# Optimization experiments

Hardware: AMD Instinct MI355X
Metric: run time of the kernel (lower is better)

## Reference

```python
import jax, jax.numpy as jnp
import numpy as np

H = 16  # num_heads
D = 64  # head_dim (latent_dim // num_heads)


def setup_inputs() -> dict:
    key = jax.random.key(0)
    ks = jax.random.split(key, 14)
    B, L, S = 2, 1024, 4096
    input_dim, latent_dim, latent_rank = 2048, 1024, 128
    sc = 0.02
    return {
        "latent": jax.random.normal(ks[0], (B, L, latent_dim), jnp.float32),
        "x": jax.random.normal(ks[1], (B, S, input_dim), jnp.float32),
        "Wq": jax.random.normal(ks[2], (latent_dim, latent_dim), jnp.float32) * sc,
        "bq": jnp.zeros((latent_dim,), jnp.float32),
        "Wc": jax.random.normal(ks[3], (input_dim, latent_rank), jnp.float32) * sc,
        "bc": jnp.zeros((latent_rank,), jnp.float32),
        "Wk": jax.random.normal(ks[4], (latent_rank, latent_dim), jnp.float32) * sc,
        "bk": jnp.zeros((latent_dim,), jnp.float32),
        "Wv": jax.random.normal(ks[5], (latent_rank, latent_dim), jnp.float32) * sc,
        "bv": jnp.zeros((latent_dim,), jnp.float32),
        "Wo": jax.random.normal(ks[6], (latent_dim, latent_dim), jnp.float32) * sc,
        "bo": jnp.zeros((latent_dim,), jnp.float32),
    }


def reference(latent, x, Wq, bq, Wc, bc, Wk, bk, Wv, bv, Wo, bo):
    B, L, latent_dim = latent.shape
    S = x.shape[1]
    # projections
    Q = latent @ Wq + bq                      # [B, L, latent_dim]
    compressed = x @ Wc + bc                  # [B, S, latent_rank] low-rank latent
    K_full = compressed @ Wk + bk             # [B, S, latent_dim]
    V_full = compressed @ Wv + bv             # [B, S, latent_dim]
    # split heads -> [B, H, len, D]
    Qh = Q.reshape(B, L, H, D).transpose(0, 2, 1, 3)
    Kh = K_full.reshape(B, S, H, D).transpose(0, 2, 1, 3)
    Vh = V_full.reshape(B, S, H, D).transpose(0, 2, 1, 3)
    scale = 1.0 / jnp.sqrt(jnp.float32(D))
    scores = jnp.einsum("bhld,bhsd->bhls", Qh, Kh) * scale  # [B,H,L,S]
    attn = jax.nn.softmax(scores, axis=-1)
    ctx = jnp.einsum("bhls,bhsd->bhld", attn, Vh)            # [B,H,L,D]
    ctx = ctx.transpose(0, 2, 1, 3).reshape(B, L, latent_dim)
    return ctx @ Wo + bo
```

## Files before the change

kernel.cpp:

```cpp
#include <hip/hip_runtime.h>
#include <hip/hip_bf16.h>

using bf16x8  = __attribute__((ext_vector_type(8))) short;
using ushort8 = __attribute__((ext_vector_type(8))) unsigned short;
using f32x4   = __attribute__((ext_vector_type(4))) float;

#define DEVINL __device__ __forceinline__

DEVINL unsigned short f2bf(float f) {
    unsigned u = __builtin_bit_cast(unsigned, f);
    u += 0x7FFFu + ((u >> 16) & 1u);
    return (unsigned short)(u >> 16);
}

DEVINL void gload_lds16(const void* g, void* l) {
    __builtin_amdgcn_global_load_lds(
        (const __attribute__((address_space(1))) void*)g,
        (__attribute__((address_space(3))) void*)l, 16, 0, 0);
}

__global__ __launch_bounds__(256) void k_convTall(
        const float* __restrict__ Wq, const float* __restrict__ Wo,
        const float* __restrict__ Wk, const float* __restrict__ Wv,
        const float* __restrict__ Wc,
        unsigned short* __restrict__ WqT, unsigned short* __restrict__ WoT,
        unsigned short* __restrict__ WkT, unsigned short* __restrict__ WvT,
        unsigned short* __restrict__ WcT) {
    __shared__ float t[32][33];
    int bx = blockIdx.x;
    const float* in; unsigned short* out; int R, C, tix;
    if (bx < 1024)      { in = Wq; out = WqT; R = 1024; C = 1024; tix = bx; }
    else if (bx < 2048) { in = Wo; out = WoT; R = 1024; C = 1024; tix = bx - 1024; }
    else if (bx < 2176) { in = Wk; out = WkT; R = 128;  C = 1024; tix = bx - 2048; }
    else if (bx < 2304) { in = Wv; out = WvT; R = 128;  C = 1024; tix = bx - 2176; }
    else                { in = Wc; out = WcT; R = 2048; C = 128;  tix = bx - 2304; }
    int ctiles = C >> 5;
    int c0 = (tix % ctiles) * 32, r0 = (tix / ctiles) * 32;
    int tx = threadIdx.x, ty = threadIdx.y;
#pragma unroll
    for (int i = 0; i < 4; i++)
        t[ty + i * 8][tx] = in[(size_t)(r0 + ty + i * 8) * C + c0 + tx];
    __syncthreads();
#pragma unroll
    for (int i = 0; i < 4; i++)
        out[(size_t)(c0 + ty + i * 8) * R + r0 + tx] = f2bf(t[tx][ty + i * 8]);
}

template <int BM, int BN, int OUTBF, int BIASROW, int AMODE>
__global__ __launch_bounds__(256) void k_gemm(const void* __restrict__ Ain,
                                              const unsigned short* __restrict__ BT,
                                              const float* __restrict__ bias,
                                              void* __restrict__ Cout,
                                              int M, int N, int K, float scale,
                                              size_t zA, size_t zB, size_t zC,
                                              const float2* __restrict__ ML) {
    constexpr int WM = BM / 2, WN = BN / 2, MI = WM / 16, NI = WN / 16;
    constexpr int CB = BN * 8 / 256;
    constexpr int CA = BM * 8 / 256;
    constexpr int EPT = BM * 64 / 256;
    constexpr int TPR = 64 / EPT;
    constexpr int NAREG = (AMODE == 2) ? EPT / 2 : (AMODE == 1 ? EPT / 4 : 1);
    __shared__ unsigned short ls[2][(BM + BN) * 64];
    const int tid = threadIdx.x, lane = tid & 63, w = tid >> 6;
    const int m0 = blockIdx.y * BM, n0 = blockIdx.x * BN, zz = blockIdx.z;
    const int mw = (w >> 1) * WM, nw = (w & 1) * WN;
    const int r16 = lane & 15, g4 = lane >> 4;
    const unsigned short* A16 = (const unsigned short*)Ain + zA * zz;
    const float* A32 = (const float*)Ain;
    BT += zB * zz;
    const int arow = tid / TPR, acol = (tid % TPR) * EPT;

    float4 areg[NAREG];
    float2 mle[2];

    f32x4 acc[MI][NI];
#pragma unroll
    for (int a = 0; a < MI; a++)
#pragma unroll
        for (int b = 0; b < NI; b++) acc[a][b] = (f32x4){0.f, 0.f, 0.f, 0.f};

    auto LOAD_A = [&](int bufi, int k0) {
        if constexpr (AMODE == 0) {
#pragma unroll
            for (int i = 0; i < CA; i++) {
                int ch = i * 256 + w * 64 + lane;
                int row = ch >> 3, c = ch & 7;
                gload_lds16(A16 + (size_t)(m0 + row) * K + k0 + c * 8,
                            &ls[bufi][(size_t)(i * 256 + w * 64) * 8]);
            }
        } else if constexpr (AMODE == 1) {
            const float* src = A32 + (size_t)(m0 + arow) * K + k0 + acol;
#pragma unroll
            for (int j = 0; j < EPT / 4; j++) areg[j] = *(const float4*)(src + j * 4);
        } else {
            const float* src = A32 + (size_t)(m0 + arow) * K + k0 + acol;
#pragma unroll
            for (int j = 0; j < EPT / 4; j++) {
                areg[j] = *(const float4*)(src + j * 4);
                areg[j + EPT / 4] = *(const float4*)(src + 2097152 + j * 4);
            }
            int b = (m0 + arow) >> 10, q = (m0 + arow) & 1023, h = k0 >> 6;
            mle[0] = ML[((size_t)(b * 16 + h)) * 1024 + q];
            mle[1] = ML[((size_t)((2 + b) * 16 + h)) * 1024 + q];
        }
    };

    auto WRITE_A = [&](int bufi) {
        if constexpr (AMODE == 1) {
            unsigned u[EPT / 2];
#pragma unroll
            for (int j = 0; j < EPT / 4; j++) {
                asm("v_cvt_pk_bf16_f32 %0, %1, %2"
                    : "=v"(u[2 * j]) : "v"(areg[j].x), "v"(areg[j].y));
                asm("v_cvt_pk_bf16_f32 %0, %1, %2"
                    : "=v"(u[2 * j + 1]) : "v"(areg[j].z), "v"(areg[j].w));
            }
#pragma unroll
            for (int j = 0; j < EPT / 8; j++)
                *(uint4*)&ls[bufi][arow * 64 + acol + j * 8] =
                    make_uint4(u[4 * j], u[4 * j + 1], u[4 * j + 2], u[4 * j + 3]);
        } else if constexpr (AMODE == 2) {
            float Mx = fmaxf(mle[0].x, mle[1].x);
            float w0 = __builtin_amdgcn_exp2f(mle[0].x - Mx);
            float w1 = __builtin_amdgcn_exp2f(mle[1].x - Mx);
            float inv = 1.f / (w0 * mle[0].y + w1 * mle[1].y);
            w0 *= inv; w1 *= inv;
            unsigned u[EPT / 2];
#pragma unroll
            for (int j = 0; j < EPT / 4; j++) {
                float4 a = areg[j], c = areg[j + EPT / 4];
                float v0 = w0 * a.x + w1 * c.x, v1 = w0 * a.y + w1 * c.y;
                float v2 = w0 * a.z + w1 * c.z, v3 = w0 * a.w + w1 * c.w;
                asm("v_cvt_pk_bf16_f32 %0, %1, %2" : "=v"(u[2 * j]) : "v"(v0), "v"(v1));
                asm("v_cvt_pk_bf16_f32 %0, %1, %2" : "=v"(u[2 * j + 1]) : "v"(v2), "v"(v3));
            }
#pragma unroll
            for (int j = 0; j < EPT / 8; j++)
                *(uint4*)&ls[bufi][arow * 64 + acol + j * 8] =
                    make_uint4(u[4 * j], u[4 * j + 1], u[4 * j + 2], u[4 * j + 3]);
        }
    };

    auto STAGE_B = [&](int bufi, int k0) {
        unsigned short* lsB = &ls[bufi][BM * 64];
#pragma unroll
        for (int i = 0; i < CB; i++) {
            int ch = i * 256 + w * 64 + lane;
            int row = ch >> 3, c = ch & 7;
            gload_lds16(BT + (size_t)(n0 + row) * K + k0 + c * 8,
                        lsB + (size_t)(i * 256 + w * 64) * 8);
        }
    };

    auto COMPUTE = [&](int bufi) {
        const unsigned short* lsA = ls[bufi];
        const unsigned short* lsB = &ls[bufi][BM * 64];
#pragma unroll
        for (int kk = 0; kk < 2; kk++) {
            bf16x8 af[MI], bfr[NI];
#pragma unroll
            for (int a = 0; a < MI; a++)
                af[a] = *(const bf16x8*)&lsA[(mw + a * 16 + r16) * 64 + kk * 32 + g4 * 8];
#pragma unroll
            for (int b = 0; b < NI; b++)
                bfr[b] = *(const bf16x8*)&lsB[(nw + b * 16 + r16) * 64 + kk * 32 + g4 * 8];
#pragma unroll
            for (int a = 0; a < MI; a++)
#pragma unroll
                for (int b = 0; b < NI; b++)
                    acc[a][b] = __builtin_amdgcn_mfma_f32_16x16x32_bf16(af[a], bfr[b], acc[a][b], 0, 0, 0);
        }
    };

    const int nk = K >> 6;
    LOAD_A(0, 0);
    STAGE_B(0, 0);
    if constexpr (AMODE != 0) WRITE_A(0);
    __syncthreads();
    for (int t = 0; t < nk; ++t) {
        int cur = t & 1, nxt = cur ^ 1;
        if (t + 1 < nk) { LOAD_A(nxt, (t + 1) << 6); STAGE_B(nxt, (t + 1) << 6); }
        COMPUTE(cur);
        if (AMODE != 0 && t + 1 < nk) WRITE_A(nxt);
        __syncthreads();
    }

#pragma unroll
    for (int b = 0; b < NI; b++) {
        int col = n0 + nw + b * 16 + r16;
        float bvc = BIASROW ? 0.f : bias[col];
#pragma unroll
        for (int a = 0; a < MI; a++) {
#pragma unroll
            for (int r = 0; r < 4; r++) {
                int row = m0 + mw + a * 16 + g4 * 4 + r;
                float bv = BIASROW ? bias[row] : bvc;
                float v = (acc[a][b][r] + bv) * scale;
                if (OUTBF)
                    ((unsigned short*)Cout)[zC * zz + (size_t)row * N + col] = f2bf(v);
                else
                    ((float*)Cout)[zC * zz + (size_t)row * N + col] = v;
            }
        }
    }
}

__global__ __launch_bounds__(256, 4) void k_attn(const unsigned short* __restrict__ Qb,
                                                 const unsigned short* __restrict__ Kb,
                                                 const unsigned short* __restrict__ VTb,
                                                 float* __restrict__ ctxp,
                                                 float2* __restrict__ ML) {
    constexpr int LD = 1024;
    constexpr float MFIX = 4.0f;
    __shared__ unsigned short lsK[2][64 * 64];
    __shared__ unsigned short lsVT[2][64 * 64];
    __shared__ unsigned short lsP[4][16 * 64];
    const int tid = threadIdx.x, lane = tid & 63, w = tid >> 6;
    const int r16 = lane & 15, g4 = lane >> 4;
    const int wg = blockIdx.x;
    const int xcd = wg & 7, t_ = wg >> 3, qi = t_ & 15, gg = t_ >> 4;
    const int g = gg * 8 + xcd;
    const int bh = g & 31, z = g >> 5;
    const int b = bh >> 4, h = bh & 15;
    const int q0 = qi * 64 + w * 16;

    const size_t qbase = ((size_t)b * 1024 + q0 + r16) * LD + h * 64;
    bf16x8 qa0 = *(const bf16x8*)&Qb[qbase + g4 * 8];
    bf16x8 qa1 = *(const bf16x8*)&Qb[qbase + 32 + g4 * 8];

    f32x4 ctxa[4];
#pragma unroll
    for (int d = 0; d < 4; d++) ctxa[d] = (f32x4){0.f, 0.f, 0.f, 0.f};
    float l_run = 0.f;

    const int s7 = r16 & 7;
    const int offk0 = r16 * 64 + ((g4 ^ s7) << 3);
    const int offk1 = r16 * 64 + (((g4 + 4) ^ s7) << 3);
    const int pwb = r16 * 64 + (g4 & 1) * 4;
    const int c2 = g4 >> 1;
    const int swn[4] = {((0 + c2) ^ s7) << 3, ((2 + c2) ^ s7) << 3,
                        ((4 + c2) ^ s7) << 3, ((6 + c2) ^ s7) << 3};

    const int lrow = lane >> 3, lcol = lane & 7;
    const int csrc = lcol ^ lrow;
    const unsigned short* gK = Kb + (size_t)b * 4096 * LD + h * 64 +
                               (size_t)(w * 8 + lrow) * LD + csrc * 8;
    const unsigned short* gV = VTb + (size_t)bh * 64 * 4096 +
                               (size_t)(w * 8 + lrow) * 4096 + csrc * 8;

    auto STAGE = [&](int bufi, int s0) {
        gload_lds16(gK + (size_t)s0 * LD, &lsK[bufi][(w * 8) * 64]);
        gload_lds16(gK + (size_t)(s0 + 32) * LD, &lsK[bufi][(32 + w * 8) * 64]);
        gload_lds16(gV + s0, &lsVT[bufi][(w * 8) * 64]);
        gload_lds16(gV + s0 + 32 * 4096, &lsVT[bufi][(32 + w * 8) * 64]);
    };

    auto COMPUTE = [&](int bufi) {
        f32x4 sc[4];
#pragma unroll
        for (int ni = 0; ni < 4; ni++) sc[ni] = (f32x4){0.f, 0.f, 0.f, 0.f};
        __builtin_amdgcn_s_setprio(1);
#pragma unroll
        for (int kk = 0; kk < 2; kk++) {
            bf16x8 qa = kk ? qa1 : qa0;
            int ofk = kk ? offk1 : offk0;
#pragma unroll
            for (int ni = 0; ni < 4; ni++) {
                bf16x8 kf = *(const bf16x8*)&lsK[bufi][ni * 1024 + ofk];
                sc[ni] = __builtin_amdgcn_mfma_f32_16x16x32_bf16(kf, qa, sc[ni], 0, 0, 0);
            }
        }
        __builtin_amdgcn_s_setprio(0);

        float pl[4];
#pragma unroll
        for (int ni = 0; ni < 4; ni++) {
            float p0 = __builtin_amdgcn_exp2f(sc[ni][0] - MFIX);
            float p1 = __builtin_amdgcn_exp2f(sc[ni][1] - MFIX);
            float p2 = __builtin_amdgcn_exp2f(sc[ni][2] - MFIX);
            float p3 = __builtin_amdgcn_exp2f(sc[ni][3] - MFIX);
            pl[ni] = (p0 + p1) + (p2 + p3);
            unsigned u0, u1;
            asm("v_cvt_pk_bf16_f32 %0, %1, %2" : "=v"(u0) : "v"(p0), "v"(p1));
            asm("v_cvt_pk_bf16_f32 %0, %1, %2" : "=v"(u1) : "v"(p2), "v"(p3));
            *(uint2*)&lsP[w][pwb + swn[ni]] = make_uint2(u0, u1);
        }
        l_run += (pl[0] + pl[1]) + (pl[2] + pl[3]);

        __builtin_amdgcn_s_setprio(1);
#pragma unroll
        for (int kk = 0; kk < 2; kk++) {
            int ofk = kk ? offk1 : offk0;
            bf16x8 pa = *(const bf16x8*)&lsP[w][ofk];
#pragma unroll
            for (int di = 0; di < 4; di++) {
                bf16x8 vf = *(const bf16x8*)&lsVT[bufi][di * 1024 + ofk];
                ctxa[di] = __builtin_amdgcn_mfma_f32_16x16x32_bf16(pa, vf, ctxa[di], 0, 0, 0);
            }
        }
        __builtin_amdgcn_s_setprio(0);
    };

    const int t0 = z * 32, t1 = t0 + 32;
    STAGE(0, t0 * 64);
    __syncthreads();
#pragma unroll 1
    for (int t = t0; t < t1; ++t) {
        int cur = (t - t0) & 1;
        if (t + 1 < t1) STAGE(cur ^ 1, (t + 1) * 64);
        COMPUTE(cur);
        __syncthreads();
    }

    l_run += __shfl_xor(l_run, 16);
    l_run += __shfl_xor(l_run, 32);

    float* cp = ctxp + ((size_t)z * 2 + b) * 1024 * 1024;
#pragma unroll
    for (int r = 0; r < 4; r++) {
        int q = q0 + g4 * 4 + r;
#pragma unroll
        for (int di = 0; di < 4; di++)
            cp[(size_t)q * 1024 + h * 64 + di * 16 + r16] = ctxa[di][r];
    }
    if (g4 == 0)
        ML[(((size_t)z * 2 + b) * 16 + h) * 1024 + q0 + r16] = make_float2(MFIX, l_run);
}

extern "C" void kernel_launch(void* const* d_in, const int* in_sizes, int n_in,
                              void* d_out, int out_size, void* d_ws, size_t ws_size,
                              hipStream_t stream) {
    const float* latent = (const float*)d_in[0];
    const float* x      = (const float*)d_in[1];
    const float* Wq     = (const float*)d_in[2];
    const float* bq     = (const float*)d_in[3];
    const float* Wc     = (const float*)d_in[4];
    const float* bc     = (const float*)d_in[5];
    const float* Wk     = (const float*)d_in[6];
    const float* bk     = (const float*)d_in[7];
    const float* Wv     = (const float*)d_in[8];
    const float* bv     = (const float*)d_in[9];
    const float* Wo     = (const float*)d_in[10];
    const float* bo     = (const float*)d_in[11];
    float* out = (float*)d_out;

    char* ws = (char*)d_ws;
    size_t off = 0;
    auto alloc = [&](size_t shorts) {
        void* p = ws + off;
        off += (shorts * 2 + 255) & ~(size_t)255;
        return (unsigned short*)p;
    };
    unsigned short* WqT  = alloc(1048576);
    unsigned short* WcT  = alloc(262144);
    unsigned short* WkT  = alloc(131072);
    unsigned short* WvT  = alloc(131072);
    unsigned short* WoT  = alloc(1048576);
    unsigned short* comp = alloc(1048576);
    unsigned short* Qb   = alloc(2097152);
    unsigned short* Kb   = alloc(8388608);
    unsigned short* VTb  = alloc(8388608);
    float*          ctxp = (float*)alloc(8388608);
    float2*         MLp  = (float2*)alloc(262144);

    k_convTall<<<2560, dim3(32, 8), 0, stream>>>(Wq, Wo, Wk, Wv, Wc,
                                                 WqT, WoT, WkT, WvT, WcT);
    k_gemm<32, 128, 1, 0, 1><<<dim3(1, 256, 1), 256, 0, stream>>>(
        x, WcT, bc, comp, 8192, 128, 2048, 1.f, 0, 0, 0, nullptr);
    k_gemm<64, 64, 1, 0, 1><<<dim3(16, 32, 1), 256, 0, stream>>>(
        latent, WqT, bq, Qb, 2048, 1024, 1024, 0.18033688f, 0, 0, 0, nullptr);
    k_gemm<128, 128, 1, 0, 0><<<dim3(8, 64, 1), 256, 0, stream>>>(
        comp, WkT, bk, Kb, 8192, 1024, 128, 1.f, 0, 0, 0, nullptr);
    k_gemm<64, 64, 1, 1, 0><<<dim3(64, 16, 2), 256, 0, stream>>>(
        WvT, comp, bv, VTb, 1024, 4096, 128, 1.f,
        0, (size_t)4096 * 128, (size_t)16 * 64 * 4096, nullptr);
    k_attn<<<1024, 256, 0, stream>>>(Qb, Kb, VTb, ctxp, MLp);
    k_gemm<64, 64, 0, 0, 2><<<dim3(16, 32, 1), 256, 0, stream>>>(
        ctxp, WoT, bo, out, 2048, 1024, 1024, 1.f, 0, 0, 0, MLp);
}
```

Before: 275.4 us.

## Use 32x32x16 MFMA in attention with register-shuffled P and separate merge kernel

```diff
diff --git a/kernel.cpp b/kernel.cpp
--- a/kernel.cpp
+++ b/kernel.cpp
@@ -4,6 +4,7 @@
 using bf16x8  = __attribute__((ext_vector_type(8))) short;
 using ushort8 = __attribute__((ext_vector_type(8))) unsigned short;
 using f32x4   = __attribute__((ext_vector_type(4))) float;
+using f32x16  = __attribute__((ext_vector_type(16))) float;
 
 #define DEVINL __device__ __forceinline__
 
@@ -17,6 +18,12 @@
     __builtin_amdgcn_global_load_lds(
         (const __attribute__((address_space(1))) void*)g,
         (__attribute__((address_space(3))) void*)l, 16, 0, 0);
+}
+
+DEVINL bf16x8 mk8(unsigned u0, unsigned u1, unsigned u2, unsigned u3) {
+    union { unsigned u[4]; bf16x8 v; } t;
+    t.u[0] = u0; t.u[1] = u1; t.u[2] = u2; t.u[3] = u3;
+    return t.v;
 }
 
 __global__ __launch_bounds__(256) void k_convTall(
@@ -52,14 +59,13 @@
                                               const float* __restrict__ bias,
                                               void* __restrict__ Cout,
                                               int M, int N, int K, float scale,
-                                              size_t zA, size_t zB, size_t zC,
-                                              const float2* __restrict__ ML) {
+                                              size_t zA, size_t zB, size_t zC) {
     constexpr int WM = BM / 2, WN = BN / 2, MI = WM / 16, NI = WN / 16;
     constexpr int CB = BN * 8 / 256;
     constexpr int CA = BM * 8 / 256;
     constexpr int EPT = BM * 64 / 256;
     constexpr int TPR = 64 / EPT;
-    constexpr int NAREG = (AMODE == 2) ? EPT / 2 : (AMODE == 1 ? EPT / 4 : 1);
+    constexpr int NAREG = (AMODE == 1) ? EPT / 4 : 1;
     __shared__ unsigned short ls[2][(BM + BN) * 64];
     const int tid = threadIdx.x, lane = tid & 63, w = tid >> 6;
     const int m0 = blockIdx.y * BM, n0 = blockIdx.x * BN, zz = blockIdx.z;
@@ -71,7 +77,6 @@
     const int arow = tid / TPR, acol = (tid % TPR) * EPT;
 
     float4 areg[NAREG];
-    float2 mle[2];
 
     f32x4 acc[MI][NI];
 #pragma unroll
@@ -88,20 +93,10 @@
                 gload_lds16(A16 + (size_t)(m0 + row) * K + k0 + c * 8,
                             &ls[bufi][(size_t)(i * 256 + w * 64) * 8]);
             }
-        } else if constexpr (AMODE == 1) {
-            const float* src = A32 + (size_t)(m0 + arow) * K + k0 + acol;
-#pragma unroll
-            for (int j = 0; j < EPT / 4; j++) areg[j] = *(const float4*)(src + j * 4);
         } else {
             const float* src = A32 + (size_t)(m0 + arow) * K + k0 + acol;
 #pragma unroll
-            for (int j = 0; j < EPT / 4; j++) {
-                areg[j] = *(const float4*)(src + j * 4);
-                areg[j + EPT / 4] = *(const float4*)(src + 2097152 + j * 4);
-            }
-            int b = (m0 + arow) >> 10, q = (m0 + arow) & 1023, h = k0 >> 6;
-            mle[0] = ML[((size_t)(b * 16 + h)) * 1024 + q];
-            mle[1] = ML[((size_t)((2 + b) * 16 + h)) * 1024 + q];
+            for (int j = 0; j < EPT / 4; j++) areg[j] = *(const float4*)(src + j * 4);
         }
     };
 
@@ -114,25 +109,6 @@
                     : "=v"(u[2 * j]) : "v"(areg[j].x), "v"(areg[j].y));
                 asm("v_cvt_pk_bf16_f32 %0, %1, %2"
                     : "=v"(u[2 * j + 1]) : "v"(areg[j].z), "v"(areg[j].w));
-            }
-#pragma unroll
-            for (int j = 0; j < EPT / 8; j++)
-                *(uint4*)&ls[bufi][arow * 64 + acol + j * 8] =
-                    make_uint4(u[4 * j], u[4 * j + 1], u[4 * j + 2], u[4 * j + 3]);
-        } else if constexpr (AMODE == 2) {
-            float Mx = fmaxf(mle[0].x, mle[1].x);
-            float w0 = __builtin_amdgcn_exp2f(mle[0].x - Mx);
-            float w1 = __builtin_amdgcn_exp2f(mle[1].x - Mx);
-            float inv = 1.f / (w0 * mle[0].y + w1 * mle[1].y);
-            w0 *= inv; w1 *= inv;
-            unsigned u[EPT / 2];
-#pragma unroll
-            for (int j = 0; j < EPT / 4; j++) {
-                float4 a = areg[j], c = areg[j + EPT / 4];
-                float v0 = w0 * a.x + w1 * c.x, v1 = w0 * a.y + w1 * c.y;
-                float v2 = w0 * a.z + w1 * c.z, v3 = w0 * a.w + w1 * c.w;
-                asm("v_cvt_pk_bf16_f32 %0, %1, %2" : "=v"(u[2 * j]) : "v"(v0), "v"(v1));
-                asm("v_cvt_pk_bf16_f32 %0, %1, %2" : "=v"(u[2 * j + 1]) : "v"(v2), "v"(v3));
             }
 #pragma unroll
             for (int j = 0; j < EPT / 8; j++)
@@ -212,91 +188,91 @@
                                                  float2* __restrict__ ML) {
     constexpr int LD = 1024;
     constexpr float MFIX = 4.0f;
-    __shared__ unsigned short lsK[2][64 * 64];
-    __shared__ unsigned short lsVT[2][64 * 64];
-    __shared__ unsigned short lsP[4][16 * 64];
+    __shared__ unsigned short lsK[2][32 * 128];
+    __shared__ unsigned short lsV[2][32 * 128];
     const int tid = threadIdx.x, lane = tid & 63, w = tid >> 6;
-    const int r16 = lane & 15, g4 = lane >> 4;
+    const int l31 = lane & 31, hi = lane >> 5;
+    const int qh = w >> 1, sh = w & 1;
     const int wg = blockIdx.x;
     const int xcd = wg & 7, t_ = wg >> 3, qi = t_ & 15, gg = t_ >> 4;
     const int g = gg * 8 + xcd;
     const int bh = g & 31, z = g >> 5;
     const int b = bh >> 4, h = bh & 15;
-    const int q0 = qi * 64 + w * 16;
-
-    const size_t qbase = ((size_t)b * 1024 + q0 + r16) * LD + h * 64;
-    bf16x8 qa0 = *(const bf16x8*)&Qb[qbase + g4 * 8];
-    bf16x8 qa1 = *(const bf16x8*)&Qb[qbase + 32 + g4 * 8];
-
-    f32x4 ctxa[4];
-#pragma unroll
-    for (int d = 0; d < 4; d++) ctxa[d] = (f32x4){0.f, 0.f, 0.f, 0.f};
+    const int q0 = qi * 64;
+
+    bf16x8 qf[4];
+    {
+        const unsigned short* qp = Qb + ((size_t)b * 1024 + q0 + qh * 32 + l31) * LD + h * 64 + hi * 8;
+#pragma unroll
+        for (int kk = 0; kk < 4; kk++) qf[kk] = *(const bf16x8*)(qp + kk * 16);
+    }
+
+    f32x16 ctx0 = {0.f,0.f,0.f,0.f,0.f,0.f,0.f,0.f,0.f,0.f,0.f,0.f,0.f,0.f,0.f,0.f};
+    f32x16 ctx1 = ctx0;
     float l_run = 0.f;
 
-    const int s7 = r16 & 7;
-    const int offk0 = r16 * 64 + ((g4 ^ s7) << 3);
-    const int offk1 = r16 * 64 + (((g4 + 4) ^ s7) << 3);
-    const int pwb = r16 * 64 + (g4 & 1) * 4;
-    const int c2 = g4 >> 1;
-    const int swn[4] = {((0 + c2) ^ s7) << 3, ((2 + c2) ^ s7) << 3,
-                        ((4 + c2) ^ s7) << 3, ((6 + c2) ^ s7) << 3};
-
-    const int lrow = lane >> 3, lcol = lane & 7;
-    const int csrc = lcol ^ lrow;
-    const unsigned short* gK = Kb + (size_t)b * 4096 * LD + h * 64 +
-                               (size_t)(w * 8 + lrow) * LD + csrc * 8;
-    const unsigned short* gV = VTb + (size_t)bh * 64 * 4096 +
-                               (size_t)(w * 8 + lrow) * 4096 + csrc * 8;
+    const int rr = lane >> 4, c16 = lane & 15;
+    const int pr0 = w * 4 + rr, pr1 = w * 4 + 16 + rr;
+    const int lc0 = c16 ^ (pr0 & 15), lc1 = c16 ^ (pr1 & 15);
+    const unsigned short* gK0 = Kb + ((size_t)b * 4096 + pr0 + (lc0 >> 3) * 32) * LD + h * 64 + (lc0 & 7) * 8;
+    const unsigned short* gK1 = Kb + ((size_t)b * 4096 + pr1 + (lc1 >> 3) * 32) * LD + h * 64 + (lc1 & 7) * 8;
+    const unsigned short* gV0 = VTb + ((size_t)bh * 64 + pr0 + (lc0 >> 3) * 32) * 4096 + (lc0 & 7) * 8;
+    const unsigned short* gV1 = VTb + ((size_t)bh * 64 + pr1 + (lc1 >> 3) * 32) * 4096 + (lc1 & 7) * 8;
+
+    int offk[4], offv[2][2];
+#pragma unroll
+    for (int kk = 0; kk < 4; kk++)
+        offk[kk] = l31 * 128 + (((sh * 8 + kk * 2 + hi) ^ (l31 & 15)) * 8);
+#pragma unroll
+    for (int ss = 0; ss < 2; ss++)
+#pragma unroll
+        for (int dh = 0; dh < 2; dh++)
+            offv[ss][dh] = l31 * 128 + (((dh * 8 + sh * 4 + ss * 2 + hi) ^ (l31 & 15)) * 8);
 
     auto STAGE = [&](int bufi, int s0) {
-        gload_lds16(gK + (size_t)s0 * LD, &lsK[bufi][(w * 8) * 64]);
-        gload_lds16(gK + (size_t)(s0 + 32) * LD, &lsK[bufi][(32 + w * 8) * 64]);
-        gload_lds16(gV + s0, &lsVT[bufi][(w * 8) * 64]);
-        gload_lds16(gV + s0 + 32 * 4096, &lsVT[bufi][(32 + w * 8) * 64]);
+        gload_lds16(gK0 + (size_t)s0 * LD, &lsK[bufi][(w * 4) * 128]);
+        gload_lds16(gK1 + (size_t)s0 * LD, &lsK[bufi][(w * 4 + 16) * 128]);
+        gload_lds16(gV0 + s0, &lsV[bufi][(w * 4) * 128]);
+        gload_lds16(gV1 + s0, &lsV[bufi][(w * 4 + 16) * 128]);
     };
 
     auto COMPUTE = [&](int bufi) {
-        f32x4 sc[4];
-#pragma unroll
-        for (int ni = 0; ni < 4; ni++) sc[ni] = (f32x4){0.f, 0.f, 0.f, 0.f};
+        f32x16 sc = {0.f,0.f,0.f,0.f,0.f,0.f,0.f,0.f,0.f,0.f,0.f,0.f,0.f,0.f,0.f,0.f};
         __builtin_amdgcn_s_setprio(1);
 #pragma unroll
-        for (int kk = 0; kk < 2; kk++) {
-            bf16x8 qa = kk ? qa1 : qa0;
-            int ofk = kk ? offk1 : offk0;
-#pragma unroll
-            for (int ni = 0; ni < 4; ni++) {
-                bf16x8 kf = *(const bf16x8*)&lsK[bufi][ni * 1024 + ofk];
-                sc[ni] = __builtin_amdgcn_mfma_f32_16x16x32_bf16(kf, qa, sc[ni], 0, 0, 0);
-            }
+        for (int kk = 0; kk < 4; kk++) {
+            bf16x8 kf = *(const bf16x8*)&lsK[bufi][offk[kk]];
+            sc = __builtin_amdgcn_mfma_f32_32x32x16_bf16(kf, qf[kk], sc, 0, 0, 0);
         }
         __builtin_amdgcn_s_setprio(0);
 
-        float pl[4];
-#pragma unroll
-        for (int ni = 0; ni < 4; ni++) {
-            float p0 = __builtin_amdgcn_exp2f(sc[ni][0] - MFIX);
-            float p1 = __builtin_amdgcn_exp2f(sc[ni][1] - MFIX);
-            float p2 = __builtin_amdgcn_exp2f(sc[ni][2] - MFIX);
-            float p3 = __builtin_amdgcn_exp2f(sc[ni][3] - MFIX);
-            pl[ni] = (p0 + p1) + (p2 + p3);
-            unsigned u0, u1;
-            asm("v_cvt_pk_bf16_f32 %0, %1, %2" : "=v"(u0) : "v"(p0), "v"(p1));
-            asm("v_cvt_pk_bf16_f32 %0, %1, %2" : "=v"(u1) : "v"(p2), "v"(p3));
-            *(uint2*)&lsP[w][pwb + swn[ni]] = make_uint2(u0, u1);
-        }
-        l_run += (pl[0] + pl[1]) + (pl[2] + pl[3]);
+        float p[16];
+#pragma unroll
+        for (int r = 0; r < 16; r++) p[r] = __builtin_amdgcn_exp2f(sc[r] - MFIX);
+        l_run += ((p[0]+p[1])+(p[2]+p[3])) + ((p[4]+p[5])+(p[6]+p[7])) +
+                 ((p[8]+p[9])+(p[10]+p[11])) + ((p[12]+p[13])+(p[14]+p[15]));
+
+        unsigned a[8];
+#pragma unroll
+        for (int j = 0; j < 8; j++)
+            asm("v_cvt_pk_bf16_f32 %0, %1, %2" : "=v"(a[j]) : "v"(p[2*j]), "v"(p[2*j+1]));
+        unsigned x1 = __shfl_xor(hi ? a[0] : a[2], 32);
+        unsigned x2 = __shfl_xor(hi ? a[1] : a[3], 32);
+        unsigned x3 = __shfl_xor(hi ? a[4] : a[6], 32);
+        unsigned x4 = __shfl_xor(hi ? a[5] : a[7], 32);
+        bf16x8 pa0 = hi ? mk8(x1, x2, a[2], a[3]) : mk8(a[0], a[1], x1, x2);
+        bf16x8 pa1 = hi ? mk8(x3, x4, a[6], a[7]) : mk8(a[4], a[5], x3, x4);
 
         __builtin_amdgcn_s_setprio(1);
-#pragma unroll
-        for (int kk = 0; kk < 2; kk++) {
-            int ofk = kk ? offk1 : offk0;
-            bf16x8 pa = *(const bf16x8*)&lsP[w][ofk];
-#pragma unroll
-            for (int di = 0; di < 4; di++) {
-                bf16x8 vf = *(const bf16x8*)&lsVT[bufi][di * 1024 + ofk];
-                ctxa[di] = __builtin_amdgcn_mfma_f32_16x16x32_bf16(pa, vf, ctxa[di], 0, 0, 0);
-            }
+        {
+            bf16x8 vb00 = *(const bf16x8*)&lsV[bufi][offv[0][0]];
+            bf16x8 vb01 = *(const bf16x8*)&lsV[bufi][offv[0][1]];
+            ctx0 = __builtin_amdgcn_mfma_f32_32x32x16_bf16(pa0, vb00, ctx0, 0, 0, 0);
+            ctx1 = __builtin_amdgcn_mfma_f32_32x32x16_bf16(pa0, vb01, ctx1, 0, 0, 0);
+            bf16x8 vb10 = *(const bf16x8*)&lsV[bufi][offv[1][0]];
+            bf16x8 vb11 = *(const bf16x8*)&lsV[bufi][offv[1][1]];
+            ctx0 = __builtin_amdgcn_mfma_f32_32x32x16_bf16(pa1, vb10, ctx0, 0, 0, 0);
+            ctx1 = __builtin_amdgcn_mfma_f32_32x32x16_bf16(pa1, vb11, ctx1, 0, 0, 0);
         }
         __builtin_amdgcn_s_setprio(0);
     };
@@ -312,19 +288,55 @@
         __syncthreads();
     }
 
-    l_run += __shfl_xor(l_run, 16);
     l_run += __shfl_xor(l_run, 32);
-
-    float* cp = ctxp + ((size_t)z * 2 + b) * 1024 * 1024;
-#pragma unroll
-    for (int r = 0; r < 4; r++) {
-        int q = q0 + g4 * 4 + r;
-#pragma unroll
-        for (int di = 0; di < 4; di++)
-            cp[(size_t)q * 1024 + h * 64 + di * 16 + r16] = ctxa[di][r];
-    }
-    if (g4 == 0)
-        ML[(((size_t)z * 2 + b) * 16 + h) * 1024 + q0 + r16] = make_float2(MFIX, l_run);
+    float* red  = (float*)&lsK[0][0];
+    float* lred = (float*)&lsV[0][0];
+    if (sh == 1) {
+#pragma unroll
+        for (int r = 0; r < 16; r++) {
+            red[qh * 2048 + r * 64 + lane] = ctx0[r];
+            red[qh * 2048 + 1024 + r * 64 + lane] = ctx1[r];
+        }
+        if (hi == 0) lred[qh * 32 + l31] = l_run;
+    }
+    __syncthreads();
+    if (sh == 0) {
+#pragma unroll
+        for (int r = 0; r < 16; r++) {
+            ctx0[r] += red[qh * 2048 + r * 64 + lane];
+            ctx1[r] += red[qh * 2048 + 1024 + r * 64 + lane];
+        }
+        l_run += lred[qh * 32 + l31];
+        float* cp = ctxp + ((size_t)z * 2 + b) * 1024 * 1024;
+#pragma unroll
+        for (int r = 0; r < 16; r++) {
+            int q = q0 + qh * 32 + (r & 3) + 8 * (r >> 2) + 4 * hi;
+            cp[(size_t)q * 1024 + h * 64 + l31] = ctx0[r];
+            cp[(size_t)q * 1024 + h * 64 + 32 + l31] = ctx1[r];
+        }
+        if (hi == 0)
+            ML[(((size_t)z * 2 + b) * 16 + h) * 1024 + q0 + qh * 32 + l31] =
+                make_float2(MFIX, l_run);
+    }
+}
+
+__global__ __launch_bounds__(256) void k_merge(const float* __restrict__ ctxp,
+                                               const float2* __restrict__ ML,
+                                               unsigned short* __restrict__ ctx) {
+    int gid = blockIdx.x * 256 + threadIdx.x;
+    int d8 = gid & 7, h = (gid >> 3) & 15, q = (gid >> 7) & 1023, b = gid >> 17;
+    float2 e0 = ML[((size_t)(b * 16 + h)) * 1024 + q];
+    float2 e1 = ML[((size_t)((2 + b) * 16 + h)) * 1024 + q];
+    float inv = 1.0f / (e0.y + e1.y);
+    const float4* p0 = (const float4*)(ctxp + (size_t)b * 1048576 + (size_t)q * 1024 + h * 64 + d8 * 8);
+    const float4* p1 = (const float4*)(ctxp + (size_t)(2 + b) * 1048576 + (size_t)q * 1024 + h * 64 + d8 * 8);
+    float4 a0 = p0[0], a1 = p0[1], c0 = p1[0], c1 = p1[1];
+    ushort8 r;
+    r[0] = f2bf((a0.x + c0.x) * inv); r[1] = f2bf((a0.y + c0.y) * inv);
+    r[2] = f2bf((a0.z + c0.z) * inv); r[3] = f2bf((a0.w + c0.w) * inv);
+    r[4] = f2bf((a1.x + c1.x) * inv); r[5] = f2bf((a1.y + c1.y) * inv);
+    r[6] = f2bf((a1.z + c1.z) * inv); r[7] = f2bf((a1.w + c1.w) * inv);
+    *(ushort8*)&ctx[((size_t)b * 1024 + q) * 1024 + h * 64 + d8 * 8] = r;
 }
 
 extern "C" void kernel_launch(void* const* d_in, const int* in_sizes, int n_in,
@@ -360,21 +372,23 @@
     unsigned short* Qb   = alloc(2097152);
     unsigned short* Kb   = alloc(8388608);
     unsigned short* VTb  = alloc(8388608);
+    unsigned short* ctxb = alloc(2097152);
     float*          ctxp = (float*)alloc(8388608);
     float2*         MLp  = (float2*)alloc(262144);
 
     k_convTall<<<2560, dim3(32, 8), 0, stream>>>(Wq, Wo, Wk, Wv, Wc,
                                                  WqT, WoT, WkT, WvT, WcT);
     k_gemm<32, 128, 1, 0, 1><<<dim3(1, 256, 1), 256, 0, stream>>>(
-        x, WcT, bc, comp, 8192, 128, 2048, 1.f, 0, 0, 0, nullptr);
+        x, WcT, bc, comp, 8192, 128, 2048, 1.f, 0, 0, 0);
     k_gemm<64, 64, 1, 0, 1><<<dim3(16, 32, 1), 256, 0, stream>>>(
-        latent, WqT, bq, Qb, 2048, 1024, 1024, 0.18033688f, 0, 0, 0, nullptr);
+        latent, WqT, bq, Qb, 2048, 1024, 1024, 0.18033688f, 0, 0, 0);
     k_gemm<128, 128, 1, 0, 0><<<dim3(8, 64, 1), 256, 0, stream>>>(
-        comp, WkT, bk, Kb, 8192, 1024, 128, 1.f, 0, 0, 0, nullptr);
+        comp, WkT, bk, Kb, 8192, 1024, 128, 1.f, 0, 0, 0);
     k_gemm<64, 64, 1, 1, 0><<<dim3(64, 16, 2), 256, 0, stream>>>(
         WvT, comp, bv, VTb, 1024, 4096, 128, 1.f,
-        0, (size_t)4096 * 128, (size_t)16 * 64 * 4096, nullptr);
+        0, (size_t)4096 * 128, (size_t)16 * 64 * 4096);
     k_attn<<<1024, 256, 0, stream>>>(Qb, Kb, VTb, ctxp, MLp);
-    k_gemm<64, 64, 0, 0, 2><<<dim3(16, 32, 1), 256, 0, stream>>>(
-        ctxp, WoT, bo, out, 2048, 1024, 1024, 1.f, 0, 0, 0, MLp);
-}
+    k_merge<<<1024, 256, 0, stream>>>(ctxp, MLp, ctxb);
+    k_gemm<64, 64, 0, 0, 0><<<dim3(16, 32, 1), 256, 0, stream>>>(
+        ctxb, WoT, bo, out, 2048, 1024, 1024, 1.f, 0, 0, 0);
+}
```

Measured after the change: 265.1 us. 1.04x faster.
